# Performance work log

Measured on AMD Instinct MI355X. Metric: run time of the kernel, lower is better.

Reference implementation:

```python
import jax, jax.numpy as jnp
import numpy as np

N_NODES = 50000
N_EDGES = 800000
N_GRAPHS = 2048


def setup_inputs() -> dict:
    key = jax.random.key(0)
    ks = jax.random.split(key, 16)
    x = jax.random.normal(ks[0], (N_NODES, 32), dtype=jnp.float32)
    edge_index = jax.random.randint(ks[1], (2, N_EDGES), 0, N_NODES, dtype=jnp.int64)
    batch = jnp.sort(jax.random.randint(ks[2], (N_NODES,), 0, N_GRAPHS, dtype=jnp.int64))
    def w(k, fi, fo):
        return jax.random.normal(k, (fi, fo), dtype=jnp.float32) * (1.0 / np.sqrt(fi))
    return {
        "x": x, "edge_index": edge_index, "batch": batch,
        "W1": w(ks[3], 32, 64), "b1": jnp.zeros((64,), jnp.float32),
        "W2": w(ks[4], 64, 64), "b2": jnp.zeros((64,), jnp.float32),
        "W3": w(ks[5], 64, 64), "b3": jnp.zeros((64,), jnp.float32),
        "lw1": w(ks[6], 64, 64), "lb1": jnp.zeros((64,), jnp.float32),
        "lw2": w(ks[7], 64, 2), "lb2": jnp.zeros((2,), jnp.float32),
    }


def reference(x, edge_index, batch, W1, b1, W2, b2, W3, b3, lw1, lb1, lw2, lb2):
    N = x.shape[0]
    # GCNConv default: add self loops, symmetric normalization
    loops = jnp.arange(N, dtype=edge_index.dtype)
    src = jnp.concatenate([edge_index[0], loops])
    dst = jnp.concatenate([edge_index[1], loops])
    ones = jnp.ones_like(src, dtype=x.dtype)
    deg = jax.ops.segment_sum(ones, dst, num_segments=N)  # in-degree incl. self loops
    dinv = jnp.where(deg > 0, jax.lax.rsqrt(deg), 0.0)
    norm = dinv[src] * dinv[dst]  # [E+N]

    def gcn_relu(h, W, b):
        h = h @ W                                    # [N, F]
        msg = h[src] * norm[:, None]                 # gather + scale [E+N, F]
        out = jax.ops.segment_sum(msg, dst, num_segments=N) + b
        return jax.nn.relu(out)

    h = gcn_relu(x, W1, b1)
    h = gcn_relu(h, W2, b2)
    h = gcn_relu(h, W3, b3)

    # global_mean_pool over graph ids
    summed = jax.ops.segment_sum(h, batch, num_segments=N_GRAPHS)  # [G, F]
    counts = jax.ops.segment_sum(jnp.ones((N,), h.dtype), batch, num_segments=N_GRAPHS)
    pooled = summed / jnp.maximum(counts, 1.0)[:, None]

    # dropout is identity in eval mode
    out = jax.nn.relu(pooled @ lw1 + lb1) @ lw2 + lb2
    return out
```

## Files before the change

kernel.cpp:

```cpp
#include <hip/hip_runtime.h>

#define NN 50000
#define NE 800000
#define NG 2048
#define F 64

constexpr int SCAN_B = 256;
constexpr int NB = (NN + SCAN_B - 1) / SCAN_B;

__global__ void deg_kernel(const int* __restrict__ dst, int* __restrict__ deg) {
    int e = blockIdx.x * 256 + threadIdx.x;
    if (e < NE) atomicAdd(&deg[dst[e]], 1);
}

__global__ void dinv_kernel(const int* __restrict__ deg, float* __restrict__ dinv) {
    int v = blockIdx.x * 256 + threadIdx.x;
    if (v < NN) dinv[v] = rsqrtf((float)(deg[v] + 1));
}

__global__ void scalex_kernel(const float4* __restrict__ x4, const float* __restrict__ dinv,
                              float4* __restrict__ xd4) {
    int i = blockIdx.x * 256 + threadIdx.x;
    if (i < NN * 8) {
        int v = i >> 3;
        float d = dinv[v];
        float4 a = x4[i];
        a.x *= d; a.y *= d; a.z *= d; a.w *= d;
        xd4[i] = a;
    }
}

__global__ void scan1_kernel(const int* __restrict__ deg, int* __restrict__ bsums) {
    __shared__ int s[256];
    int t = threadIdx.x, i = blockIdx.x * 256 + t;
    s[t] = (i < NN) ? deg[i] : 0;
    __syncthreads();
    for (int off = 128; off > 0; off >>= 1) {
        if (t < off) s[t] += s[t + off];
        __syncthreads();
    }
    if (t == 0) bsums[blockIdx.x] = s[0];
}

__global__ void scan2_kernel(int* __restrict__ bsums, int* __restrict__ rowptr) {
    __shared__ int s[256];
    int t = threadIdx.x;
    int v = (t < NB) ? bsums[t] : 0;
    s[t] = v;
    __syncthreads();
    for (int off = 1; off < 256; off <<= 1) {
        int x = (t >= off) ? s[t - off] : 0;
        __syncthreads();
        s[t] += x;
        __syncthreads();
    }
    if (t < NB) bsums[t] = s[t] - v;
    if (t == 0) rowptr[NN] = NE;
}

__global__ void scan3_kernel(const int* __restrict__ deg, const int* __restrict__ bsums,
                             int* __restrict__ rowptr, int* __restrict__ cursor) {
    __shared__ int s[256];
    int t = threadIdx.x, i = blockIdx.x * 256 + t;
    int v = (i < NN) ? deg[i] : 0;
    s[t] = v;
    __syncthreads();
    for (int off = 1; off < 256; off <<= 1) {
        int x = (t >= off) ? s[t - off] : 0;
        __syncthreads();
        s[t] += x;
        __syncthreads();
    }
    if (i < NN) {
        int rp = bsums[blockIdx.x] + s[t] - v;
        rowptr[i] = rp;
        cursor[i] = rp;
    }
}

__global__ void fill_kernel(const int* __restrict__ src, const int* __restrict__ dst,
                            int* __restrict__ cursor, int* __restrict__ col) {
    int e = blockIdx.x * 256 + threadIdx.x;
    if (e < NE) {
        int slot = atomicAdd(&cursor[dst[e]], 1);
        col[slot] = src[e];
    }
}

__global__ void agg32_kernel(const float4* __restrict__ g4, const int* __restrict__ rowptr,
                             const int* __restrict__ col, const float* __restrict__ dinv,
                             float4* __restrict__ out4) {
    int lane = threadIdx.x & 63;
    int v = blockIdx.x * 4 + (threadIdx.x >> 6);
    int slot = lane >> 3, fq = lane & 7;
    int beg = rowptr[v], end = rowptr[v + 1];
    float4 acc = {0.f, 0.f, 0.f, 0.f};
    for (int base = beg; base < end; base += 32) {
        float4 a[4];
        float w[4];
#pragma unroll
        for (int j = 0; j < 4; ++j) {
            int e = base + slot + j * 8;
            int ce = (e < end) ? e : (end - 1);
            w[j] = (e < end) ? 1.f : 0.f;
            int u = col[ce];
            a[j] = g4[(long)u * 8 + fq];
        }
#pragma unroll
        for (int j = 0; j < 4; ++j) {
            acc.x = fmaf(w[j], a[j].x, acc.x);
            acc.y = fmaf(w[j], a[j].y, acc.y);
            acc.z = fmaf(w[j], a[j].z, acc.z);
            acc.w = fmaf(w[j], a[j].w, acc.w);
        }
    }
#pragma unroll
    for (int m = 8; m < 64; m <<= 1) {
        acc.x += __shfl_xor(acc.x, m);
        acc.y += __shfl_xor(acc.y, m);
        acc.z += __shfl_xor(acc.z, m);
        acc.w += __shfl_xor(acc.w, m);
    }
    float4 self = g4[(long)v * 8 + fq];
    float d = dinv[v];
    acc.x = d * (acc.x + self.x);
    acc.y = d * (acc.y + self.y);
    acc.z = d * (acc.z + self.z);
    acc.w = d * (acc.w + self.w);
    if (slot == 0) out4[(long)v * 8 + fq] = acc;
}

template <bool POOL>
__global__ void agg4_kernel(const float4* __restrict__ g4, const int* __restrict__ rowptr,
                            const int* __restrict__ col, const float* __restrict__ dinv,
                            const float4* __restrict__ bias4, float4* __restrict__ out4,
                            const int* __restrict__ batch, float* __restrict__ pooled,
                            float* __restrict__ counts) {
    int lane = threadIdx.x & 63;
    int v = blockIdx.x * 4 + (threadIdx.x >> 6);
    int slot = lane >> 4, fq = lane & 15;
    int beg = rowptr[v], end = rowptr[v + 1];
    float4 acc = {0.f, 0.f, 0.f, 0.f};
    for (int base = beg; base < end; base += 32) {
        float4 a[8];
        float w[8];
#pragma unroll
        for (int j = 0; j < 8; ++j) {
            int e = base + slot + j * 4;
            int ce = (e < end) ? e : (end - 1);
            w[j] = (e < end) ? 1.f : 0.f;
            int u = col[ce];
            a[j] = g4[(long)u * 16 + fq];
        }
#pragma unroll
        for (int j = 0; j < 8; ++j) {
            acc.x = fmaf(w[j], a[j].x, acc.x);
            acc.y = fmaf(w[j], a[j].y, acc.y);
            acc.z = fmaf(w[j], a[j].z, acc.z);
            acc.w = fmaf(w[j], a[j].w, acc.w);
        }
    }
#pragma unroll
    for (int m = 16; m < 64; m <<= 1) {
        acc.x += __shfl_xor(acc.x, m);
        acc.y += __shfl_xor(acc.y, m);
        acc.z += __shfl_xor(acc.z, m);
        acc.w += __shfl_xor(acc.w, m);
    }
    float4 self = g4[(long)v * 16 + fq];
    float d = dinv[v];
    float4 bb = bias4[fq];
    float4 hv;
    hv.x = fmaxf(fmaf(d, acc.x + self.x, bb.x), 0.f);
    hv.y = fmaxf(fmaf(d, acc.y + self.y, bb.y), 0.f);
    hv.z = fmaxf(fmaf(d, acc.z + self.z, bb.z), 0.f);
    hv.w = fmaxf(fmaf(d, acc.w + self.w, bb.w), 0.f);
    if (slot == 0) {
        if (POOL) {
            int b = batch[v];
            float* p = pooled + (long)b * F + fq * 4;
            atomicAdd(p + 0, hv.x);
            atomicAdd(p + 1, hv.y);
            atomicAdd(p + 2, hv.z);
            atomicAdd(p + 3, hv.w);
            if (lane == 0) atomicAdd(&counts[b], 1.0f);
        } else {
            out4[(long)v * 16 + fq] = hv;
        }
    }
}

template <int K, bool RELU_BIAS>
__global__ void gemm_kernel(const float* __restrict__ in, const float* __restrict__ W,
                            const float* __restrict__ bias, const float* __restrict__ dinv,
                            float* __restrict__ out) {
    __shared__ float Ws[K * F];
    int t = threadIdx.x;
#pragma unroll
    for (int i = 0; i < K * F / 256; ++i) Ws[i * 256 + t] = W[i * 256 + t];
    __syncthreads();
    int f = t & 63;
    int slot = __builtin_amdgcn_readfirstlane(t >> 6);
    int n0 = blockIdx.x * 16 + slot;
    float acc0 = 0.f, acc1 = 0.f, acc2 = 0.f, acc3 = 0.f;
    const float* r0 = in + (long)n0 * K;
    const float* r1 = r0 + 4 * K;
    const float* r2 = r0 + 8 * K;
    const float* r3 = r0 + 12 * K;
#pragma unroll
    for (int k = 0; k < K; ++k) {
        float w = Ws[k * F + f];
        acc0 = fmaf(r0[k], w, acc0);
        acc1 = fmaf(r1[k], w, acc1);
        acc2 = fmaf(r2[k], w, acc2);
        acc3 = fmaf(r3[k], w, acc3);
    }
    if (RELU_BIAS) {
        float b = bias[f];
        out[(long)n0 * F + f]        = fmaxf(acc0 + b, 0.f);
        out[(long)(n0 + 4) * F + f]  = fmaxf(acc1 + b, 0.f);
        out[(long)(n0 + 8) * F + f]  = fmaxf(acc2 + b, 0.f);
        out[(long)(n0 + 12) * F + f] = fmaxf(acc3 + b, 0.f);
    } else {
        out[(long)n0 * F + f]        = dinv[n0] * acc0;
        out[(long)(n0 + 4) * F + f]  = dinv[n0 + 4] * acc1;
        out[(long)(n0 + 8) * F + f]  = dinv[n0 + 8] * acc2;
        out[(long)(n0 + 12) * F + f] = dinv[n0 + 12] * acc3;
    }
}

__global__ void head_kernel(const float* __restrict__ pooled, const float* __restrict__ counts,
                            const float* __restrict__ lw1, const float* __restrict__ lb1,
                            const float* __restrict__ lw2, const float* __restrict__ lb2,
                            float* __restrict__ out) {
    __shared__ float p[F];
    __shared__ float hid[F];
    int gid = blockIdx.x, t = threadIdx.x;
    float cnt = fmaxf(counts[gid], 1.0f);
    p[t] = pooled[(long)gid * F + t] / cnt;
    __syncthreads();
    float acc = lb1[t];
#pragma unroll 8
    for (int k = 0; k < F; ++k) acc = fmaf(p[k], lw1[k * F + t], acc);
    hid[t] = fmaxf(acc, 0.f);
    __syncthreads();
    if (t < 2) {
        float a = lb2[t];
#pragma unroll 8
        for (int k = 0; k < F; ++k) a = fmaf(hid[k], lw2[k * 2 + t], a);
        out[(long)gid * 2 + t] = a;
    }
}

extern "C" void kernel_launch(void* const* d_in, const int* in_sizes, int n_in,
                              void* d_out, int out_size, void* d_ws, size_t ws_size,
                              hipStream_t stream) {
    const float* x    = (const float*)d_in[0];
    const int*   ei   = (const int*)d_in[1];
    const int*   bat  = (const int*)d_in[2];
    const float* W1   = (const float*)d_in[3];
    const float* b1   = (const float*)d_in[4];
    const float* W2   = (const float*)d_in[5];
    const float* b2   = (const float*)d_in[6];
    const float* W3   = (const float*)d_in[7];
    const float* b3   = (const float*)d_in[8];
    const float* lw1  = (const float*)d_in[9];
    const float* lb1  = (const float*)d_in[10];
    const float* lw2  = (const float*)d_in[11];
    const float* lb2  = (const float*)d_in[12];
    float* out = (float*)d_out;

    const int* src = ei;
    const int* dst = ei + NE;

    char* ws = (char*)d_ws;
    size_t off = 0;
    auto carve = [&](size_t bytes) {
        void* p = ws + off;
        off += (bytes + 255) & ~(size_t)255;
        return p;
    };
    int*   deg     = (int*)carve(NN * 4);
    float* dinv    = (float*)carve(NN * 4);
    int*   rowptr  = (int*)carve((NN + 1) * 4);
    int*   cursor  = (int*)carve(NN * 4);
    int*   bsums   = (int*)carve(256 * 4);
    int*   col     = (int*)carve((size_t)NE * 4);
    float* xd      = (float*)carve((size_t)NN * 32 * 4);
    float* sbuf    = (float*)carve((size_t)NN * 32 * 4);
    float* bufA    = (float*)carve((size_t)NN * F * 4);
    float* bufB    = (float*)carve((size_t)NN * F * 4);
    float* pooled  = (float*)carve((size_t)NG * F * 4 + NG * 4);
    float* counts  = pooled + (size_t)NG * F;

    hipMemsetAsync(deg, 0, NN * 4, stream);
    hipMemsetAsync(pooled, 0, ((size_t)NG * F + NG) * 4, stream);

    deg_kernel<<<(NE + 255) / 256, 256, 0, stream>>>(dst, deg);
    dinv_kernel<<<NB, 256, 0, stream>>>(deg, dinv);
    scalex_kernel<<<(NN * 8 + 255) / 256, 256, 0, stream>>>((const float4*)x, dinv, (float4*)xd);
    scan1_kernel<<<NB, 256, 0, stream>>>(deg, bsums);
    scan2_kernel<<<1, 256, 0, stream>>>(bsums, rowptr);
    scan3_kernel<<<NB, 256, 0, stream>>>(deg, bsums, rowptr, cursor);
    fill_kernel<<<(NE + 255) / 256, 256, 0, stream>>>(src, dst, cursor, col);

    const int gridN = (NN + 3) / 4;
    const int gridG = NN / 16;

    agg32_kernel<<<gridN, 256, 0, stream>>>((const float4*)xd, rowptr, col, dinv, (float4*)sbuf);
    gemm_kernel<32, true><<<gridG, 256, 0, stream>>>(sbuf, W1, b1, dinv, bufA);

    gemm_kernel<64, false><<<gridG, 256, 0, stream>>>(bufA, W2, nullptr, dinv, bufB);
    agg4_kernel<false><<<gridN, 256, 0, stream>>>((const float4*)bufB, rowptr, col, dinv,
                                                  (const float4*)b2, (float4*)bufA,
                                                  nullptr, nullptr, nullptr);
    gemm_kernel<64, false><<<gridG, 256, 0, stream>>>(bufA, W3, nullptr, dinv, bufB);
    agg4_kernel<true><<<gridN, 256, 0, stream>>>((const float4*)bufB, rowptr, col, dinv,
                                                 (const float4*)b3, nullptr,
                                                 bat, pooled, counts);
    head_kernel<<<NG, 64, 0, stream>>>(pooled, counts, lw1, lb1, lw2, lb2, out);
}
```

Before: 348.3 us.

## Split CSR aggregation into source-node blocks for cache-resident gather passes

Edges are bucketed by destination and by source block (four blocks of 12500 nodes), and each aggregation is split into four passes, each gathering only from one source block. The intent is to keep the gathered feature slice in L2/MALL cache across a pass. Partial sums are carried between passes through nontemporal loads and stores of the accumulator. The cost is four times as many launches, a larger scan over 200k entries, extra accumulator traffic, and less unrolling in the inner gather loop.

```diff
diff --git a/kernel.cpp b/kernel.cpp
--- a/kernel.cpp
+++ b/kernel.cpp
@@ -4,18 +4,36 @@
 #define NE 800000
 #define NG 2048
 #define F 64
-
-constexpr int SCAN_B = 256;
-constexpr int NB = (NN + SCAN_B - 1) / SCAN_B;
-
-__global__ void deg_kernel(const int* __restrict__ dst, int* __restrict__ deg) {
+#define SBLK 4
+#define SRCDIV 12500
+#define M2 (NN * SBLK)
+
+constexpr int NB2 = (M2 + 255) / 256;
+
+typedef float f4 __attribute__((ext_vector_type(4)));
+
+static __device__ __forceinline__ f4 ntload(const f4* p) {
+    return __builtin_nontemporal_load(p);
+}
+static __device__ __forceinline__ void ntstore(f4* p, f4 v) {
+    __builtin_nontemporal_store(v, p);
+}
+
+__global__ void deg2_kernel(const int* __restrict__ src, const int* __restrict__ dst,
+                            int* __restrict__ deg2) {
     int e = blockIdx.x * 256 + threadIdx.x;
-    if (e < NE) atomicAdd(&deg[dst[e]], 1);
-}
-
-__global__ void dinv_kernel(const int* __restrict__ deg, float* __restrict__ dinv) {
+    if (e < NE) {
+        int blk = src[e] / SRCDIV;
+        atomicAdd(&deg2[dst[e] * SBLK + blk], 1);
+    }
+}
+
+__global__ void dinv_kernel(const int* __restrict__ deg2, float* __restrict__ dinv) {
     int v = blockIdx.x * 256 + threadIdx.x;
-    if (v < NN) dinv[v] = rsqrtf((float)(deg[v] + 1));
+    if (v < NN) {
+        const int4 d4 = ((const int4*)deg2)[v];
+        dinv[v] = rsqrtf((float)(d4.x + d4.y + d4.z + d4.w + 1));
+    }
 }
 
 __global__ void scalex_kernel(const float4* __restrict__ x4, const float* __restrict__ dinv,
@@ -30,10 +48,10 @@
     }
 }
 
-__global__ void scan1_kernel(const int* __restrict__ deg, int* __restrict__ bsums) {
+__global__ void scan1_kernel(const int* __restrict__ deg2, int* __restrict__ bsums) {
     __shared__ int s[256];
     int t = threadIdx.x, i = blockIdx.x * 256 + t;
-    s[t] = (i < NN) ? deg[i] : 0;
+    s[t] = (i < M2) ? deg2[i] : 0;
     __syncthreads();
     for (int off = 128; off > 0; off >>= 1) {
         if (t < off) s[t] += s[t + off];
@@ -42,10 +60,27 @@
     if (t == 0) bsums[blockIdx.x] = s[0];
 }
 
-__global__ void scan2_kernel(int* __restrict__ bsums, int* __restrict__ rowptr) {
+__global__ void scan2_kernel(int* __restrict__ bsums, int* __restrict__ rowptr2) {
+    __shared__ int s[1024];
+    int t = threadIdx.x;
+    int v = (t < NB2) ? bsums[t] : 0;
+    s[t] = v;
+    __syncthreads();
+    for (int off = 1; off < 1024; off <<= 1) {
+        int x = (t >= off) ? s[t - off] : 0;
+        __syncthreads();
+        s[t] += x;
+        __syncthreads();
+    }
+    if (t < NB2) bsums[t] = s[t] - v;
+    if (t == 0) rowptr2[M2] = NE;
+}
+
+__global__ void scan3_kernel(const int* __restrict__ deg2, const int* __restrict__ bsums,
+                             int* __restrict__ rowptr2, int* __restrict__ cursor2) {
     __shared__ int s[256];
-    int t = threadIdx.x;
-    int v = (t < NB) ? bsums[t] : 0;
+    int t = threadIdx.x, i = blockIdx.x * 256 + t;
+    int v = (i < M2) ? deg2[i] : 0;
     s[t] = v;
     __syncthreads();
     for (int off = 1; off < 256; off <<= 1) {
@@ -54,138 +89,109 @@
         s[t] += x;
         __syncthreads();
     }
-    if (t < NB) bsums[t] = s[t] - v;
-    if (t == 0) rowptr[NN] = NE;
-}
-
-__global__ void scan3_kernel(const int* __restrict__ deg, const int* __restrict__ bsums,
-                             int* __restrict__ rowptr, int* __restrict__ cursor) {
-    __shared__ int s[256];
-    int t = threadIdx.x, i = blockIdx.x * 256 + t;
-    int v = (i < NN) ? deg[i] : 0;
-    s[t] = v;
-    __syncthreads();
-    for (int off = 1; off < 256; off <<= 1) {
-        int x = (t >= off) ? s[t - off] : 0;
-        __syncthreads();
-        s[t] += x;
-        __syncthreads();
-    }
-    if (i < NN) {
+    if (i < M2) {
         int rp = bsums[blockIdx.x] + s[t] - v;
-        rowptr[i] = rp;
-        cursor[i] = rp;
+        rowptr2[i] = rp;
+        cursor2[i] = rp;
     }
 }
 
 __global__ void fill_kernel(const int* __restrict__ src, const int* __restrict__ dst,
-                            int* __restrict__ cursor, int* __restrict__ col) {
+                            int* __restrict__ cursor2, int* __restrict__ col) {
     int e = blockIdx.x * 256 + threadIdx.x;
     if (e < NE) {
-        int slot = atomicAdd(&cursor[dst[e]], 1);
-        col[slot] = src[e];
-    }
-}
-
-__global__ void agg32_kernel(const float4* __restrict__ g4, const int* __restrict__ rowptr,
-                             const int* __restrict__ col, const float* __restrict__ dinv,
-                             float4* __restrict__ out4) {
+        int s = src[e];
+        int slot = atomicAdd(&cursor2[dst[e] * SBLK + s / SRCDIV], 1);
+        col[slot] = s;
+    }
+}
+
+template <bool FIRST, bool LAST>
+__global__ void agg32_pass(const f4* __restrict__ g4, const int* __restrict__ rowptr2,
+                           const int* __restrict__ col, const float* __restrict__ dinv,
+                           f4* __restrict__ acc4, int p) {
     int lane = threadIdx.x & 63;
     int v = blockIdx.x * 4 + (threadIdx.x >> 6);
     int slot = lane >> 3, fq = lane & 7;
-    int beg = rowptr[v], end = rowptr[v + 1];
-    float4 acc = {0.f, 0.f, 0.f, 0.f};
-    for (int base = beg; base < end; base += 32) {
-        float4 a[4];
-        float w[4];
-#pragma unroll
-        for (int j = 0; j < 4; ++j) {
-            int e = base + slot + j * 8;
-            int ce = (e < end) ? e : (end - 1);
-            w[j] = (e < end) ? 1.f : 0.f;
-            int u = col[ce];
-            a[j] = g4[(long)u * 8 + fq];
-        }
-#pragma unroll
-        for (int j = 0; j < 4; ++j) {
-            acc.x = fmaf(w[j], a[j].x, acc.x);
-            acc.y = fmaf(w[j], a[j].y, acc.y);
-            acc.z = fmaf(w[j], a[j].z, acc.z);
-            acc.w = fmaf(w[j], a[j].w, acc.w);
-        }
+    long rowbase = (long)v * 8 + fq;
+    f4 prev = FIRST ? g4[rowbase] : ntload(&acc4[rowbase]);
+    int beg = rowptr2[v * SBLK + p], end = rowptr2[v * SBLK + p + 1];
+    f4 part = {0.f, 0.f, 0.f, 0.f};
+    for (int base = beg; base < end; base += 8) {
+        int e = base + slot;
+        int ce = (e < end) ? e : end - 1;
+        float w = (e < end) ? 1.f : 0.f;
+        int u = col[ce];
+        part += w * g4[(long)u * 8 + fq];
     }
 #pragma unroll
     for (int m = 8; m < 64; m <<= 1) {
-        acc.x += __shfl_xor(acc.x, m);
-        acc.y += __shfl_xor(acc.y, m);
-        acc.z += __shfl_xor(acc.z, m);
-        acc.w += __shfl_xor(acc.w, m);
-    }
-    float4 self = g4[(long)v * 8 + fq];
-    float d = dinv[v];
-    acc.x = d * (acc.x + self.x);
-    acc.y = d * (acc.y + self.y);
-    acc.z = d * (acc.z + self.z);
-    acc.w = d * (acc.w + self.w);
-    if (slot == 0) out4[(long)v * 8 + fq] = acc;
-}
-
-template <bool POOL>
-__global__ void agg4_kernel(const float4* __restrict__ g4, const int* __restrict__ rowptr,
-                            const int* __restrict__ col, const float* __restrict__ dinv,
-                            const float4* __restrict__ bias4, float4* __restrict__ out4,
-                            const int* __restrict__ batch, float* __restrict__ pooled,
-                            float* __restrict__ counts) {
+        part.x += __shfl_xor(part.x, m);
+        part.y += __shfl_xor(part.y, m);
+        part.z += __shfl_xor(part.z, m);
+        part.w += __shfl_xor(part.w, m);
+    }
+    f4 val = prev + part;
+    if (!LAST) {
+        if (slot == 0) ntstore(&acc4[rowbase], val);
+    } else {
+        if (slot == 0) acc4[rowbase] = dinv[v] * val;
+    }
+}
+
+template <bool FIRST, bool LAST, bool POOL>
+__global__ void agg4_pass(const f4* __restrict__ g4, const int* __restrict__ rowptr2,
+                          const int* __restrict__ col, const float* __restrict__ dinv,
+                          const f4* __restrict__ bias4, f4* __restrict__ acc4, int p,
+                          const int* __restrict__ batch, float* __restrict__ pooled,
+                          float* __restrict__ counts) {
     int lane = threadIdx.x & 63;
     int v = blockIdx.x * 4 + (threadIdx.x >> 6);
     int slot = lane >> 4, fq = lane & 15;
-    int beg = rowptr[v], end = rowptr[v + 1];
-    float4 acc = {0.f, 0.f, 0.f, 0.f};
-    for (int base = beg; base < end; base += 32) {
-        float4 a[8];
-        float w[8];
-#pragma unroll
-        for (int j = 0; j < 8; ++j) {
+    long rowbase = (long)v * 16 + fq;
+    f4 prev = FIRST ? g4[rowbase] : ntload(&acc4[rowbase]);
+    int beg = rowptr2[v * SBLK + p], end = rowptr2[v * SBLK + p + 1];
+    f4 part = {0.f, 0.f, 0.f, 0.f};
+    for (int base = beg; base < end; base += 8) {
+#pragma unroll
+        for (int j = 0; j < 2; ++j) {
             int e = base + slot + j * 4;
-            int ce = (e < end) ? e : (end - 1);
-            w[j] = (e < end) ? 1.f : 0.f;
+            int ce = (e < end) ? e : end - 1;
+            float w = (e < end) ? 1.f : 0.f;
             int u = col[ce];
-            a[j] = g4[(long)u * 16 + fq];
+            part += w * g4[(long)u * 16 + fq];
         }
-#pragma unroll
-        for (int j = 0; j < 8; ++j) {
-            acc.x = fmaf(w[j], a[j].x, acc.x);
-            acc.y = fmaf(w[j], a[j].y, acc.y);
-            acc.z = fmaf(w[j], a[j].z, acc.z);
-            acc.w = fmaf(w[j], a[j].w, acc.w);
-        }
     }
 #pragma unroll
     for (int m = 16; m < 64; m <<= 1) {
-        acc.x += __shfl_xor(acc.x, m);
-        acc.y += __shfl_xor(acc.y, m);
-        acc.z += __shfl_xor(acc.z, m);
-        acc.w += __shfl_xor(acc.w, m);
-    }
-    float4 self = g4[(long)v * 16 + fq];
-    float d = dinv[v];
-    float4 bb = bias4[fq];
-    float4 hv;
-    hv.x = fmaxf(fmaf(d, acc.x + self.x, bb.x), 0.f);
-    hv.y = fmaxf(fmaf(d, acc.y + self.y, bb.y), 0.f);
-    hv.z = fmaxf(fmaf(d, acc.z + self.z, bb.z), 0.f);
-    hv.w = fmaxf(fmaf(d, acc.w + self.w, bb.w), 0.f);
-    if (slot == 0) {
-        if (POOL) {
-            int b = batch[v];
-            float* p = pooled + (long)b * F + fq * 4;
-            atomicAdd(p + 0, hv.x);
-            atomicAdd(p + 1, hv.y);
-            atomicAdd(p + 2, hv.z);
-            atomicAdd(p + 3, hv.w);
-            if (lane == 0) atomicAdd(&counts[b], 1.0f);
-        } else {
-            out4[(long)v * 16 + fq] = hv;
+        part.x += __shfl_xor(part.x, m);
+        part.y += __shfl_xor(part.y, m);
+        part.z += __shfl_xor(part.z, m);
+        part.w += __shfl_xor(part.w, m);
+    }
+    f4 val = prev + part;
+    if (!LAST) {
+        if (slot == 0) ntstore(&acc4[rowbase], val);
+    } else {
+        float d = dinv[v];
+        f4 bb = bias4[fq];
+        f4 hv;
+        hv.x = fmaxf(fmaf(d, val.x, bb.x), 0.f);
+        hv.y = fmaxf(fmaf(d, val.y, bb.y), 0.f);
+        hv.z = fmaxf(fmaf(d, val.z, bb.z), 0.f);
+        hv.w = fmaxf(fmaf(d, val.w, bb.w), 0.f);
+        if (slot == 0) {
+            if (POOL) {
+                int b = batch[v];
+                float* pp = pooled + (long)b * F + fq * 4;
+                atomicAdd(pp + 0, hv.x);
+                atomicAdd(pp + 1, hv.y);
+                atomicAdd(pp + 2, hv.z);
+                atomicAdd(pp + 3, hv.w);
+                if (lane == 0) atomicAdd(&counts[b], 1.0f);
+            } else {
+                acc4[rowbase] = hv;
+            }
         }
     }
 }
@@ -280,11 +286,11 @@
         off += (bytes + 255) & ~(size_t)255;
         return p;
     };
-    int*   deg     = (int*)carve(NN * 4);
+    int*   deg2    = (int*)carve((size_t)M2 * 4);
     float* dinv    = (float*)carve(NN * 4);
-    int*   rowptr  = (int*)carve((NN + 1) * 4);
-    int*   cursor  = (int*)carve(NN * 4);
-    int*   bsums   = (int*)carve(256 * 4);
+    int*   rowptr2 = (int*)carve((size_t)(M2 + 1) * 4);
+    int*   cursor2 = (int*)carve((size_t)M2 * 4);
+    int*   bsums   = (int*)carve(1024 * 4);
     int*   col     = (int*)carve((size_t)NE * 4);
     float* xd      = (float*)carve((size_t)NN * 32 * 4);
     float* sbuf    = (float*)carve((size_t)NN * 32 * 4);
@@ -293,30 +299,45 @@
     float* pooled  = (float*)carve((size_t)NG * F * 4 + NG * 4);
     float* counts  = pooled + (size_t)NG * F;
 
-    hipMemsetAsync(deg, 0, NN * 4, stream);
+    hipMemsetAsync(deg2, 0, (size_t)M2 * 4, stream);
     hipMemsetAsync(pooled, 0, ((size_t)NG * F + NG) * 4, stream);
 
-    deg_kernel<<<(NE + 255) / 256, 256, 0, stream>>>(dst, deg);
-    dinv_kernel<<<NB, 256, 0, stream>>>(deg, dinv);
+    deg2_kernel<<<(NE + 255) / 256, 256, 0, stream>>>(src, dst, deg2);
+    dinv_kernel<<<(NN + 255) / 256, 256, 0, stream>>>(deg2, dinv);
     scalex_kernel<<<(NN * 8 + 255) / 256, 256, 0, stream>>>((const float4*)x, dinv, (float4*)xd);
-    scan1_kernel<<<NB, 256, 0, stream>>>(deg, bsums);
-    scan2_kernel<<<1, 256, 0, stream>>>(bsums, rowptr);
-    scan3_kernel<<<NB, 256, 0, stream>>>(deg, bsums, rowptr, cursor);
-    fill_kernel<<<(NE + 255) / 256, 256, 0, stream>>>(src, dst, cursor, col);
+    scan1_kernel<<<NB2, 256, 0, stream>>>(deg2, bsums);
+    scan2_kernel<<<1, 1024, 0, stream>>>(bsums, rowptr2);
+    scan3_kernel<<<NB2, 256, 0, stream>>>(deg2, bsums, rowptr2, cursor2);
+    fill_kernel<<<(NE + 255) / 256, 256, 0, stream>>>(src, dst, cursor2, col);
 
     const int gridN = (NN + 3) / 4;
     const int gridG = NN / 16;
 
-    agg32_kernel<<<gridN, 256, 0, stream>>>((const float4*)xd, rowptr, col, dinv, (float4*)sbuf);
+    agg32_pass<true,  false><<<gridN, 256, 0, stream>>>((const f4*)xd, rowptr2, col, dinv, (f4*)sbuf, 0);
+    agg32_pass<false, false><<<gridN, 256, 0, stream>>>((const f4*)xd, rowptr2, col, dinv, (f4*)sbuf, 1);
+    agg32_pass<false, false><<<gridN, 256, 0, stream>>>((const f4*)xd, rowptr2, col, dinv, (f4*)sbuf, 2);
+    agg32_pass<false, true ><<<gridN, 256, 0, stream>>>((const f4*)xd, rowptr2, col, dinv, (f4*)sbuf, 3);
     gemm_kernel<32, true><<<gridG, 256, 0, stream>>>(sbuf, W1, b1, dinv, bufA);
 
     gemm_kernel<64, false><<<gridG, 256, 0, stream>>>(bufA, W2, nullptr, dinv, bufB);
-    agg4_kernel<false><<<gridN, 256, 0, stream>>>((const float4*)bufB, rowptr, col, dinv,
-                                                  (const float4*)b2, (float4*)bufA,
-                                                  nullptr, nullptr, nullptr);
+    agg4_pass<true,  false, false><<<gridN, 256, 0, stream>>>((const f4*)bufB, rowptr2, col, dinv,
+                                                              (const f4*)b2, (f4*)bufA, 0, nullptr, nullptr, nullptr);
+    agg4_pass<false, false, false><<<gridN, 256, 0, stream>>>((const f4*)bufB, rowptr2, col, dinv,
+                                                              (const f4*)b2, (f4*)bufA, 1, nullptr, nullptr, nullptr);
+    agg4_pass<false, false, false><<<gridN, 256, 0, stream>>>((const f4*)bufB, rowptr2, col, dinv,
+                                                              (const f4*)b2, (f4*)bufA, 2, nullptr, nullptr, nullptr);
+    agg4_pass<false, true,  false><<<gridN, 256, 0, stream>>>((const f4*)bufB, rowptr2, col, dinv,
+                                                              (const f4*)b2, (f4*)bufA, 3, nullptr, nullptr, nullptr);
+
     gemm_kernel<64, false><<<gridG, 256, 0, stream>>>(bufA, W3, nullptr, dinv, bufB);
-    agg4_kernel<true><<<gridN, 256, 0, stream>>>((const float4*)bufB, rowptr, col, dinv,
-                                                 (const float4*)b3, nullptr,
-                                                 bat, pooled, counts);
+    agg4_pass<true,  false, false><<<gridN, 256, 0, stream>>>((const f4*)bufB, rowptr2, col, dinv,
+                                                              (const f4*)b3, (f4*)bufA, 0, nullptr, nullptr, nullptr);
+    agg4_pass<false, false, false><<<gridN, 256, 0, stream>>>((const f4*)bufB, rowptr2, col, dinv,
+                                                              (const f4*)b3, (f4*)bufA, 1, nullptr, nullptr, nullptr);
+    agg4_pass<false, false, false><<<gridN, 256, 0, stream>>>((const f4*)bufB, rowptr2, col, dinv,
+                                                              (const f4*)b3, (f4*)bufA, 2, nullptr, nullptr, nullptr);
+    agg4_pass<false, true,  true ><<<gridN, 256, 0, stream>>>((const f4*)bufB, rowptr2, col, dinv,
+                                                              (const f4*)b3, (f4*)bufA, 3, bat, pooled, counts);
+
     head_kernel<<<NG, 64, 0, stream>>>(pooled, counts, lw1, lb1, lw2, lb2, out);
 }
```

New measurement: 464.5 us. +33.4%, slower.
